# Kernel tuning notes

Hardware: AMD Instinct MI355X
Metric: run time of the kernel (lower is better)

## Reference

```python
import jax, jax.numpy as jnp
import numpy as np

HEADS = 12
D_MODEL = 768
D_K = D_MODEL // HEADS
BS, SEQ = 2, 4096


def setup_inputs() -> dict:
    key = jax.random.key(0)
    ks = jax.random.split(key, 12)
    s = 1.0 / np.sqrt(D_MODEL)
    return {
        "q": jax.random.normal(ks[0], (BS, SEQ, D_MODEL), jnp.float32),
        "k": jax.random.normal(ks[1], (BS, SEQ, D_MODEL), jnp.float32),
        "v": jax.random.normal(ks[2], (BS, SEQ, D_MODEL), jnp.float32),
        "Wq": jax.random.normal(ks[3], (D_MODEL, D_MODEL), jnp.float32) * s,
        "bq": jax.random.normal(ks[4], (D_MODEL,), jnp.float32) * s,
        "Wk": jax.random.normal(ks[5], (D_MODEL, D_MODEL), jnp.float32) * s,
        "bk": jax.random.normal(ks[6], (D_MODEL,), jnp.float32) * s,
        "Wv": jax.random.normal(ks[7], (D_MODEL, D_MODEL), jnp.float32) * s,
        "bv": jax.random.normal(ks[8], (D_MODEL,), jnp.float32) * s,
        "Wo": jax.random.normal(ks[9], (D_MODEL, D_MODEL), jnp.float32) * s,
        "bo": jax.random.normal(ks[10], (D_MODEL,), jnp.float32) * s,
        "mask": jnp.ones((BS, 1, SEQ), jnp.int32),
    }


def reference(q, k, v, Wq, bq, Wk, bk, Wv, bv, Wo, bo, mask):
    bs, sq, _ = q.shape
    # torch Linear: x @ W.T + b; then reshape to (bs, S, h, d_k) and transpose to (bs, h, S, d_k)
    def proj(x, W, b):
        y = x @ W.T + b
        return y.reshape(bs, -1, HEADS, D_K).transpose(0, 2, 1, 3)
    qh, kh, vh = proj(q, Wq, bq), proj(k, Wk, bk), proj(v, Wv, bv)
    scores = jnp.einsum("bhqd,bhkd->bhqk", qh, kh) / np.sqrt(D_K)
    # mask.unsqueeze(1): [bs,1,1,S_kv], masked_fill where mask == 0
    scores = jnp.where(mask[:, None, :, :] == 0, jnp.float32(-1e9), scores)
    attn = jax.nn.softmax(scores, axis=-1)  # dropout = identity (eval mode)
    ctx = jnp.einsum("bhqk,bhkd->bhqd", attn, vh)
    concat = ctx.transpose(0, 2, 1, 3).reshape(bs, sq, D_MODEL)
    return concat @ Wo.T + bo
```

## Files before the change

kernel.cpp:

```cpp
#include <hip/hip_runtime.h>
#include <hip/hip_bf16.h>

typedef __bf16 bf16x8 __attribute__((ext_vector_type(8)));
typedef __bf16 bf16x4 __attribute__((ext_vector_type(4)));
typedef float f32x4 __attribute__((ext_vector_type(4)));
typedef unsigned short u16;

#define HEADS 12
#define DK 64
#define DM 768
#define SEQL 4096
#define BSZ 2
#define MROWS (BSZ * SEQL)
#define WELEM (DM * DM)
#define NX 6291456
#define WTOT (4 * WELEM)
#define BTOT (4 * 768)

#define QSCALE 0.180336880434245f
#define EXP2F(x) __builtin_amdgcn_exp2f(x)

__device__ __forceinline__ float bf2f(u16 x) {
    unsigned int u = ((unsigned int)x) << 16;
    return __uint_as_float(u);
}
__device__ __forceinline__ u16 f2bf(float f) {
    unsigned int u = __float_as_uint(f);
    u += 0x7fff + ((u >> 16) & 1);
    return (u16)(u >> 16);
}
__device__ __forceinline__ unsigned int cvt_pk(float lo, float hi) {
#if __has_builtin(__builtin_amdgcn_cvt_pk_bf16_f32)
    auto r = __builtin_amdgcn_cvt_pk_bf16_f32(lo, hi);
    unsigned int u;
    __builtin_memcpy(&u, &r, 4);
    return u;
#else
    return (unsigned int)f2bf(lo) | ((unsigned int)f2bf(hi) << 16);
#endif
}

__global__ void detect_dtype(const u16* __restrict__ q, int* __restrict__ flag) {
    __shared__ int cnt;
    if (threadIdx.x == 0) cnt = 0;
    __syncthreads();
    int c = 0;
    for (int i = threadIdx.x; i < 16384; i += 256) {
        u16 x = q[i];
        if (((x >> 7) & 0xFF) == 0xFF) c++;
    }
    if (c) atomicAdd(&cnt, c);
    __syncthreads();
    if (threadIdx.x == 0) *flag = (cnt > 0) ? 1 : 0;
}

#define XBLKS (3 * NX / 8 / 256)
#define WBBLKS (((WTOT + BTOT) / 4 + 255) / 256)
__global__ __launch_bounds__(256) void convert_all(
    const void* __restrict__ X0, const void* __restrict__ X1, const void* __restrict__ X2,
    const void* __restrict__ W0, const void* __restrict__ W1,
    const void* __restrict__ W2, const void* __restrict__ W3,
    const void* __restrict__ B0, const void* __restrict__ B1,
    const void* __restrict__ B2, const void* __restrict__ B3,
    u16* __restrict__ Xc, u16* __restrict__ Wc, u16* __restrict__ bc,
    const int* __restrict__ flag) {
    const int f32m = *flag;
    if (blockIdx.x < XBLKS) {
        int i8 = blockIdx.x * 256 + threadIdx.x;
        int w = i8 / (NX / 8);
        int off8 = i8 - w * (NX / 8);
        const void* src = (w == 0) ? X0 : (w == 1) ? X1 : X2;
        u16* dst = Xc + (size_t)w * NX + (size_t)off8 * 8;
        if (f32m) {
            float4 f0 = ((const float4*)src)[off8 * 2];
            float4 f1 = ((const float4*)src)[off8 * 2 + 1];
            uint4 p = {cvt_pk(f0.x, f0.y), cvt_pk(f0.z, f0.w),
                       cvt_pk(f1.x, f1.y), cvt_pk(f1.z, f1.w)};
            *(uint4*)dst = p;
        } else {
            *(uint4*)dst = ((const uint4*)src)[off8];
        }
        return;
    }
    int i4 = (blockIdx.x - XBLKS) * 256 + threadIdx.x;
    const int n4 = (WTOT + BTOT) / 4;
    if (i4 >= n4) return;
    int base = i4 * 4;
    const void* src;
    u16* dst;
    int off;
    if (base < WTOT) {
        int w = base / WELEM;
        off = base - w * WELEM;
        src = (w == 0) ? W0 : (w == 1) ? W1 : (w == 2) ? W2 : W3;
        dst = Wc + w * WELEM + off;
    } else {
        int bi = base - WTOT;
        int w = bi / 768;
        off = bi - w * 768;
        src = (w == 0) ? B0 : (w == 1) ? B1 : (w == 2) ? B2 : B3;
        dst = bc + w * 768 + off;
    }
    if (f32m) {
        float4 f = *(const float4*)((const float*)src + off);
        uint2 p = {cvt_pk(f.x, f.y), cvt_pk(f.z, f.w)};
        *(uint2*)dst = p;
    } else {
        *(uint2*)dst = *(const uint2*)((const u16*)src + off);
    }
}

typedef __attribute__((address_space(1))) unsigned int glb_u32;
typedef __attribute__((address_space(3))) unsigned int lds_u32;

__device__ __forceinline__ void gld16(const u16* g, u16* l) {
    __builtin_amdgcn_global_load_lds((glb_u32*)g, (lds_u32*)l, 16, 0, 0);
}

template <int NCH>
__device__ __forceinline__ void stage_g(const u16* gbase, u16* lbase, int tid) {
#pragma unroll
    for (int it = 0; it < NCH / 256; ++it) {
        int c = it * 256 + tid;
        int row = c >> 2, p = c & 3;
        int gc = p ^ (row & 3);
        gld16(gbase + (size_t)row * DM + gc * 8, lbase + c * 8);
    }
}

__global__ __launch_bounds__(256) void gemm_qkv3(
    const u16* __restrict__ X0, const u16* __restrict__ X1, const u16* __restrict__ X2,
    const u16* __restrict__ Wc, const u16* __restrict__ bc,
    u16* __restrict__ Yq, u16* __restrict__ Yk, u16* __restrict__ Yv) {
    __shared__ __align__(16) u16 SM[2][2][128 * 32];

    const int L   = blockIdx.y * 64 + blockIdx.x;
    const int g   = L >> 3;
    const int bxn = (L & 7) * 8 + (g & 7);
    const int byn = g >> 3;

    const int sel = byn / 6;
    const int n0  = (byn - sel * 6) * 128;
    const int m0  = bxn * 128;

    const u16* X  = sel == 0 ? X0 : (sel == 1 ? X1 : X2);
    const u16* W  = Wc + (size_t)sel * WELEM;
    const u16* Bp = bc + sel * 768;
    u16* Y = sel == 0 ? Yq : (sel == 1 ? Yk : Yv);
    const float oscale = sel == 0 ? QSCALE : 1.0f;

    const int tid = threadIdx.x, lane = tid & 63, wave = tid >> 6;
    const int wr = (wave >> 1) * 64, wc2 = (wave & 1) * 64;
    const int l15 = lane & 15, quad = lane >> 4;
    const int ck = (quad ^ (l15 & 3)) * 8;

    f32x4 acc[4][4] = {};

    stage_g<512>(X + (size_t)m0 * DM, &SM[0][0][0], tid);
    stage_g<512>(W + (size_t)n0 * DM, &SM[1][0][0], tid);
    __syncthreads();

    for (int it = 0; it < 24; ++it) {
        const int cur = it & 1, nxt = cur ^ 1;
        if (it < 23) {
            stage_g<512>(X + (size_t)m0 * DM + (it + 1) * 32, &SM[0][nxt][0], tid);
            stage_g<512>(W + (size_t)n0 * DM + (it + 1) * 32, &SM[1][nxt][0], tid);
        }
        bf16x8 a[4], b[4];
#pragma unroll
        for (int i = 0; i < 4; ++i)
            a[i] = *(const bf16x8*)&SM[0][cur][(wr + i * 16 + l15) * 32 + ck];
#pragma unroll
        for (int j = 0; j < 4; ++j)
            b[j] = *(const bf16x8*)&SM[1][cur][(wc2 + j * 16 + l15) * 32 + ck];
        if (sel < 2) {
#pragma unroll
            for (int i = 0; i < 4; ++i)
#pragma unroll
                for (int j = 0; j < 4; ++j)
                    acc[i][j] = __builtin_amdgcn_mfma_f32_16x16x32_bf16(b[j], a[i], acc[i][j], 0, 0, 0);
        } else {
#pragma unroll
            for (int i = 0; i < 4; ++i)
#pragma unroll
                for (int j = 0; j < 4; ++j)
                    acc[i][j] = __builtin_amdgcn_mfma_f32_16x16x32_bf16(a[i], b[j], acc[i][j], 0, 0, 0);
        }
        __syncthreads();
    }

    u16* eb = &SM[0][0][0] + wave * 4096;
    const int r7l = l15 & 7;
    const int hh = (n0 + wc2) >> 6;

    if (sel < 2) {
        f32x4 bj[4];
#pragma unroll
        for (int j = 0; j < 4; ++j) {
            uint2 bb4 = *(const uint2*)&Bp[n0 + wc2 + j * 16 + quad * 4];
            bj[j][0] = bf2f((u16)(bb4.x & 0xffff));
            bj[j][1] = bf2f((u16)(bb4.x >> 16));
            bj[j][2] = bf2f((u16)(bb4.y & 0xffff));
            bj[j][3] = bf2f((u16)(bb4.y >> 16));
        }
#pragma unroll
        for (int i = 0; i < 4; ++i) {
            int Yl = i * 16 + l15;
#pragma unroll
            for (int j = 0; j < 4; ++j) {
                float v0 = (acc[i][j][0] + bj[j][0]) * oscale;
                float v1 = (acc[i][j][1] + bj[j][1]) * oscale;
                float v2 = (acc[i][j][2] + bj[j][2]) * oscale;
                float v3 = (acc[i][j][3] + bj[j][3]) * oscale;
                uint2 cv = {cvt_pk(v0, v1), cvt_pk(v2, v3)};
                int ch = (j * 4 + quad) ^ (r7l * 2);
                *(uint2*)&eb[Yl * 64 + ch * 4] = cv;
            }
        }
        asm volatile("" ::: "memory");
#pragma unroll
        for (int it2 = 0; it2 < 8; ++it2) {
            int Yp = it2 * 8 + (lane >> 3);
            int sc = ((lane & 7) * 2) ^ ((Yp & 7) * 2);
            uint4 w = *(const uint4*)&eb[Yp * 64 + sc * 4];
            int row0 = m0 + wr + Yp;
            int bb = row0 >> 12, s0 = row0 & (SEQL - 1);
            *(uint4*)&Y[(((size_t)(bb * HEADS + hh)) << 18) + (s0 << 6) + (lane & 7) * 8] = w;
        }
    } else {
#pragma unroll
        for (int j = 0; j < 4; ++j) {
            int Yl = j * 16 + l15;
            float bv = bf2f(Bp[n0 + wc2 + Yl]);
#pragma unroll
            for (int i = 0; i < 4; ++i) {
                uint2 cv = {cvt_pk(acc[i][j][0] + bv, acc[i][j][1] + bv),
                            cvt_pk(acc[i][j][2] + bv, acc[i][j][3] + bv)};
                int ch = (i * 4 + quad) ^ (r7l * 2);
                *(uint2*)&eb[Yl * 64 + ch * 4] = cv;
            }
        }
        asm volatile("" ::: "memory");
        const int bb = (m0 + wr) >> 12, s0 = (m0 + wr) & (SEQL - 1);
#pragma unroll
        for (int it2 = 0; it2 < 8; ++it2) {
            int Yp = it2 * 8 + (lane >> 3);
            int sc = ((lane & 7) * 2) ^ ((Yp & 7) * 2);
            uint4 w = *(const uint4*)&eb[Yp * 64 + sc * 4];
            *(uint4*)&Y[(((size_t)(bb * HEADS + hh)) << 18) + ((size_t)Yp << 12) + s0 + (lane & 7) * 8] = w;
        }
    }
}

__global__ __launch_bounds__(256) void gemm_out3(const u16* __restrict__ X,
                                                 const u16* __restrict__ W,
                                                 const u16* __restrict__ Bp,
                                                 void* __restrict__ Y,
                                                 const int* __restrict__ flag) {
    __shared__ __align__(16) u16 As[2][64 * 32];
    __shared__ __align__(16) u16 Bs[2][128 * 32];

    const int f32mode = *flag;
    const int L  = blockIdx.y * 128 + blockIdx.x;
    const int g  = L >> 3;
    const int m0 = ((L & 7) * 16 + (g & 15)) * 64;
    const int n0 = (g >> 4) * 128;
    const int tid = threadIdx.x, lane = tid & 63, wave = tid >> 6;
    const int wr = (wave >> 1) * 32, wc2 = (wave & 1) * 64;
    const int l15 = lane & 15, quad = lane >> 4;
    const int ck = (quad ^ (l15 & 3)) * 8;

    f32x4 acc[2][4] = {};

    stage_g<256>(X + (size_t)m0 * DM, &As[0][0], tid);
    stage_g<512>(W + (size_t)n0 * DM, &Bs[0][0], tid);
    __syncthreads();

    for (int it = 0; it < 24; ++it) {
        const int cur = it & 1, nxt = cur ^ 1;
        if (it < 23) {
            stage_g<256>(X + (size_t)m0 * DM + (it + 1) * 32, &As[nxt][0], tid);
            stage_g<512>(W + (size_t)n0 * DM + (it + 1) * 32, &Bs[nxt][0], tid);
        }
        bf16x8 a[2], b[4];
#pragma unroll
        for (int i = 0; i < 2; ++i)
            a[i] = *(const bf16x8*)&As[cur][(wr + i * 16 + l15) * 32 + ck];
#pragma unroll
        for (int j = 0; j < 4; ++j)
            b[j] = *(const bf16x8*)&Bs[cur][(wc2 + j * 16 + l15) * 32 + ck];
#pragma unroll
        for (int i = 0; i < 2; ++i)
#pragma unroll
            for (int j = 0; j < 4; ++j)
                acc[i][j] = __builtin_amdgcn_mfma_f32_16x16x32_bf16(a[i], b[j], acc[i][j], 0, 0, 0);
        __syncthreads();
    }

#pragma unroll
    for (int j = 0; j < 4; ++j) {
        int o = n0 + wc2 + j * 16 + l15;
        float bv = bf2f(Bp[o]);
#pragma unroll
        for (int i = 0; i < 2; ++i)
#pragma unroll
            for (int r = 0; r < 4; ++r) {
                int row = m0 + wr + i * 16 + quad * 4 + r;
                float val = acc[i][j][r] + bv;
                if (f32mode) ((float*)Y)[(size_t)row * DM + o] = val;
                else         ((u16*)Y)[(size_t)row * DM + o] = f2bf(val);
            }
    }
}

__device__ __forceinline__ void stage8_bf16(u16* dst, const u16* src) {
    *(uint4*)dst = *(const uint4*)src;
}
__device__ __forceinline__ void stage16_bf16(u16* dst, const u16* src) {
    *(uint4*)dst = *(const uint4*)src;
    *(uint4*)(dst + 8) = *(const uint4*)(src + 8);
}
__device__ __forceinline__ void stage16_f32pk(u16* dst, const float* src) {
    float4 f0 = ((const float4*)src)[0];
    float4 f1 = ((const float4*)src)[1];
    float4 f2 = ((const float4*)src)[2];
    float4 f3 = ((const float4*)src)[3];
    uint4 lo = {cvt_pk(f0.x, f0.y), cvt_pk(f0.z, f0.w), cvt_pk(f1.x, f1.y), cvt_pk(f1.z, f1.w)};
    uint4 hi = {cvt_pk(f2.x, f2.y), cvt_pk(f2.z, f2.w), cvt_pk(f3.x, f3.y), cvt_pk(f3.z, f3.w)};
    *(uint4*)dst = lo;
    *(uint4*)(dst + 8) = hi;
}

__global__ __launch_bounds__(256) void gemm_qkv_fb(
    const void* __restrict__ Xq, const void* __restrict__ Xk, const void* __restrict__ Xv,
    const u16* __restrict__ Wc, const u16* __restrict__ bc,
    u16* __restrict__ Yq, u16* __restrict__ Yk, u16* __restrict__ Yv,
    const int* __restrict__ flag) {
    __shared__ __align__(16) u16 As[128][40];
    __shared__ __align__(16) u16 Bs[64][40];
    const int f32mode = *flag;
    const int by = blockIdx.y;
    const int sel = by / 12;
    const int n0 = (by - sel * 12) * 64;
    const int m0 = blockIdx.x * 128;
    const void* Xp = sel == 0 ? Xq : (sel == 1 ? Xk : Xv);
    const u16* Wp = Wc + sel * WELEM;
    const u16* Bp = bc + sel * 768;
    u16* Y = sel == 0 ? Yq : (sel == 1 ? Yk : Yv);
    const float oscale = sel == 0 ? QSCALE : 1.0f;
    const int tid = threadIdx.x, lane = tid & 63, wave = tid >> 6;
    const int wr = (wave >> 1) * 64, wc = (wave & 1) * 32;
    const int l15 = lane & 15, quad = lane >> 4;
    const int srA = tid >> 1, scA = (tid & 1) * 16;
    const int srB = tid >> 2, scB = (tid & 3) * 8;
    f32x4 acc[4][2] = {};
    const size_t xoff = (size_t)(m0 + srA) * DM + scA;
    const size_t woff = (size_t)(n0 + srB) * DM + scB;
    for (int kb = 0; kb < DM; kb += 32) {
        if (f32mode) stage16_f32pk(&As[srA][scA], (const float*)Xp + xoff + kb);
        else         stage16_bf16(&As[srA][scA], (const u16*)Xp + xoff + kb);
        stage8_bf16(&Bs[srB][scB], Wp + woff + kb);
        __syncthreads();
        bf16x8 a[4], b[2];
#pragma unroll
        for (int i = 0; i < 4; ++i) a[i] = *(const bf16x8*)&As[wr + i * 16 + l15][quad * 8];
#pragma unroll
        for (int j = 0; j < 2; ++j) b[j] = *(const bf16x8*)&Bs[wc + j * 16 + l15][quad * 8];
#pragma unroll
        for (int i = 0; i < 4; ++i)
#pragma unroll
            for (int j = 0; j < 2; ++j)
                acc[i][j] = __builtin_amdgcn_mfma_f32_16x16x32_bf16(a[i], b[j], acc[i][j], 0, 0, 0);
        __syncthreads();
    }
#pragma unroll
    for (int j = 0; j < 2; ++j) {
        int o = n0 + wc + j * 16 + l15;
        float bv = bf2f(Bp[o]);
#pragma unroll
        for (int i = 0; i < 4; ++i)
#pragma unroll
            for (int r = 0; r < 4; ++r) {
                int row = m0 + wr + i * 16 + quad * 4 + r;
                float val = (acc[i][j][r] + bv) * oscale;
                int bb = row >> 12, s = row & (SEQL - 1);
                int h = o >> 6, d = o & 63;
                if (sel < 2) Y[((bb * HEADS + h) << 18) + (s << 6) + d] = f2bf(val);
                else         Y[((bb * HEADS + h) << 18) + (d << 12) + s] = f2bf(val);
            }
    }
}

__global__ __launch_bounds__(256) void gemm_out_fb(const u16* __restrict__ X,
                                                   const u16* __restrict__ Wp,
                                                   const u16* __restrict__ Bp,
                                                   void* __restrict__ Y,
                                                   const int* __restrict__ flag) {
    __shared__ __align__(16) u16 As[128][40];
    __shared__ __align__(16) u16 Bs[64][40];
    const int f32mode = *flag;
    const int m0 = blockIdx.x * 128, n0 = blockIdx.y * 64;
    const int tid = threadIdx.x, lane = tid & 63, wave = tid >> 6;
    const int wr = (wave >> 1) * 64, wc = (wave & 1) * 32;
    const int l15 = lane & 15, quad = lane >> 4;
    const int srA = tid >> 1, scA = (tid & 1) * 16;
    const int srB = tid >> 2, scB = (tid & 3) * 8;
    f32x4 acc[4][2] = {};
    const size_t xoff = (size_t)(m0 + srA) * DM + scA;
    const size_t woff = (size_t)(n0 + srB) * DM + scB;
    for (int kb = 0; kb < DM; kb += 32) {
        stage16_bf16(&As[srA][scA], X + xoff + kb);
        stage8_bf16(&Bs[srB][scB], Wp + woff + kb);
        __syncthreads();
        bf16x8 a[4], b[2];
#pragma unroll
        for (int i = 0; i < 4; ++i) a[i] = *(const bf16x8*)&As[wr + i * 16 + l15][quad * 8];
#pragma unroll
        for (int j = 0; j < 2; ++j) b[j] = *(const bf16x8*)&Bs[wc + j * 16 + l15][quad * 8];
#pragma unroll
        for (int i = 0; i < 4; ++i)
#pragma unroll
            for (int j = 0; j < 2; ++j)
                acc[i][j] = __builtin_amdgcn_mfma_f32_16x16x32_bf16(a[i], b[j], acc[i][j], 0, 0, 0);
        __syncthreads();
    }
#pragma unroll
    for (int j = 0; j < 2; ++j) {
        int o = n0 + wc + j * 16 + l15;
        float bv = bf2f(Bp[o]);
#pragma unroll
        for (int i = 0; i < 4; ++i)
#pragma unroll
            for (int r = 0; r < 4; ++r) {
                int row = m0 + wr + i * 16 + quad * 4 + r;
                float val = acc[i][j][r] + bv;
                if (f32mode) ((float*)Y)[(size_t)row * DM + o] = val;
                else         ((u16*)Y)[(size_t)row * DM + o] = f2bf(val);
            }
    }
}

__device__ __forceinline__ void stage_tile(const u16* gbase, int rstride,
                                           u16* lbase, int tid) {
#pragma unroll
    for (int it = 0; it < 2; ++it) {
        int c = it * 256 + tid;
        int row = c >> 3, p = c & 7;
        int gc = p ^ (row & 7);
        gld16(gbase + (size_t)row * rstride + gc * 8, lbase + c * 8);
    }
}

__global__ __launch_bounds__(256, 3) void flash_attn(const u16* __restrict__ Q,
                                                     const u16* __restrict__ K,
                                                     const u16* __restrict__ Vt,
                                                     const int* __restrict__ mask,
                                                     u16* __restrict__ ctx) {
    __shared__ __align__(16) u16 KVs[2][2][64 * 64];
    __shared__ __align__(16) float Ms[2][64];
    __shared__ int Mf[2];
    __shared__ int AnyM;

    const int tid  = threadIdx.x;
    const int lane = tid & 63;
    const int wave = tid >> 6;
    const int l15  = lane & 15;
    const int quad = lane >> 4;

    const int L  = blockIdx.y * 32 + blockIdx.x;
    const int gg = L >> 3;
    const int bh = (L & 7) * 3 + (gg >> 5);
    const int qblk = gg & 31;

    const int b  = bh / HEADS;
    const int h  = bh - b * HEADS;
    const int qb = qblk * 128 + wave * 32;

    const u16* Qh = Q  + ((size_t)bh << 18);
    const u16* Kh = K  + ((size_t)bh << 18);
    const u16* Vh = Vt + ((size_t)bh << 18);
    const int* maskb = mask + b * SEQL;

    if (tid == 0) AnyM = 0;
    int zf = 0;
#pragma unroll
    for (int i = 0; i < 16; ++i) zf |= (maskb[tid + i * 256] == 0);

    bf16x8 aq[2][2];
#pragma unroll
    for (int s = 0; s < 2; ++s)
#pragma unroll
        for (int c = 0; c < 2; ++c)
            aq[s][c] = *(const bf16x8*)&Qh[(size_t)(qb + s * 16 + l15) * DK + c * 32 + quad * 8];

    __syncthreads();
    if (zf) atomicOr(&AnyM, 1);
    __syncthreads();
    const int anym = AnyM;

    const int r7   = l15 & 7;
    const int ck0  = (quad ^ r7) * 8;
    const int ck1  = ((quad + 4) ^ r7) * 8;
    const int lrow = l15 * 64;
    const int vq   = quad >> 1;
    const int voff = (quad & 1) * 4;

    f32x4 o_acc[2][4] = {};
    f32x4 l_acc[2] = {};

    bf16x8 aones;
    {
        unsigned int w1 = 0x3F803F80u;
        uint4 o4 = {w1, w1, w1, w1};
        __builtin_memcpy(&aones, &o4, 16);
    }

    stage_tile(Kh, DK, &KVs[0][0][0], tid);
    stage_tile(Vh, SEQL, &KVs[0][1][0], tid);
    int mreg = 0;
    if (anym && tid < 64) {
        mreg = maskb[tid];
        int anyt = __any(mreg == 0);
        Ms[0][tid] = (mreg == 0) ? -1.0e9f : 0.0f;
        if (tid == 0) Mf[0] = anyt;
        mreg = maskb[64 + tid];
    }
    __syncthreads();

#pragma unroll 2
    for (int t = 0; t < 64; ++t) {
        const int cur = t & 1, nxt = cur ^ 1;
        if (t < 63) {
            const int kt = (t + 1) * 64;
            stage_tile(Kh + (size_t)kt * DK, DK, &KVs[nxt][0][0], tid);
            stage_tile(Vh + kt, SEQL, &KVs[nxt][1][0], tid);
            if (anym && tid < 64) {
                int anyt = __any(mreg == 0);
                Ms[nxt][tid] = (mreg == 0) ? -1.0e9f : 0.0f;
                if (tid == 0) Mf[nxt] = anyt;
                if (t < 62) mreg = maskb[(t + 2) * 64 + tid];
            }
        }

        const u16* kb2 = &KVs[cur][0][0];
        const u16* vb  = &KVs[cur][1][0];

        f32x4 s4[2][4];
#pragma unroll
        for (int nt = 0; nt < 4; ++nt) {
            bf16x8 ak0 = *(const bf16x8*)&kb2[lrow + nt * 1024 + ck0];
            bf16x8 ak1 = *(const bf16x8*)&kb2[lrow + nt * 1024 + ck1];
#pragma unroll
            for (int s = 0; s < 2; ++s) {
                f32x4 z = {};
                z = __builtin_amdgcn_mfma_f32_16x16x32_bf16(ak0, aq[s][0], z, 0, 0, 0);
                z = __builtin_amdgcn_mfma_f32_16x16x32_bf16(ak1, aq[s][1], z, 0, 0, 0);
                s4[s][nt] = z;
            }
        }
        const int usebias = anym ? Mf[cur] : 0;
        if (usebias) {
#pragma unroll
            for (int nt = 0; nt < 4; ++nt) {
                f32x4 bias = *(const f32x4*)&Ms[cur][nt * 16 + quad * 4];
#pragma unroll
                for (int s = 0; s < 2; ++s)
#pragma unroll
                    for (int r = 0; r < 4; ++r) s4[s][nt][r] += bias[r];
            }
        }

#pragma unroll
        for (int s = 0; s < 2; ++s)
#pragma unroll
            for (int nt = 0; nt < 4; ++nt) {
                s4[s][nt][0] = EXP2F(s4[s][nt][0]);
                s4[s][nt][1] = EXP2F(s4[s][nt][1]);
                s4[s][nt][2] = EXP2F(s4[s][nt][2]);
                s4[s][nt][3] = EXP2F(s4[s][nt][3]);
            }

        bf16x8 pp[2][2];
#pragma unroll
        for (int s = 0; s < 2; ++s)
#pragma unroll
            for (int kbi = 0; kbi < 2; ++kbi) {
                uint4 cv = {cvt_pk(s4[s][2 * kbi][0],     s4[s][2 * kbi][1]),
                            cvt_pk(s4[s][2 * kbi][2],     s4[s][2 * kbi][3]),
                            cvt_pk(s4[s][2 * kbi + 1][0], s4[s][2 * kbi + 1][1]),
                            cvt_pk(s4[s][2 * kbi + 1][2], s4[s][2 * kbi + 1][3])};
                __builtin_memcpy(&pp[s][kbi], &cv, 16);
            }

        bf16x8 av[4][2];
#pragma unroll
        for (int dv = 0; dv < 4; ++dv) {
            const u16* vr = &vb[(dv * 16 + l15) * 64];
#pragma unroll
            for (int kbi = 0; kbi < 2; ++kbi) {
                uint2 lo = *(const uint2*)&vr[((kbi * 4 + vq) ^ r7) * 8 + voff];
                uint2 hi = *(const uint2*)&vr[((kbi * 4 + 2 + vq) ^ r7) * 8 + voff];
                uint4 cc = {lo.x, lo.y, hi.x, hi.y};
                __builtin_memcpy(&av[dv][kbi], &cc, 16);
            }
        }

        __builtin_amdgcn_s_setprio(1);
#pragma unroll
        for (int kbi = 0; kbi < 2; ++kbi) {
#pragma unroll
            for (int dv = 0; dv < 4; ++dv)
#pragma unroll
                for (int s = 0; s < 2; ++s)
                    o_acc[s][dv] = __builtin_amdgcn_mfma_f32_16x16x32_bf16(
                        av[dv][kbi], pp[s][kbi], o_acc[s][dv], 0, 0, 0);
#pragma unroll
            for (int s = 0; s < 2; ++s)
                l_acc[s] = __builtin_amdgcn_mfma_f32_16x16x32_bf16(
                    aones, pp[s][kbi], l_acc[s], 0, 0, 0);
        }
        __builtin_amdgcn_s_setprio(0);
        __syncthreads();
    }

    u16* eb = &KVs[0][0][0] + wave * 2304;
#pragma unroll
    for (int s = 0; s < 2; ++s) {
        float inv = 1.0f / l_acc[s][0];
#pragma unroll
        for (int dv = 0; dv < 4; ++dv) {
            uint2 cv = {cvt_pk(o_acc[s][dv][0] * inv, o_acc[s][dv][1] * inv),
                        cvt_pk(o_acc[s][dv][2] * inv, o_acc[s][dv][3] * inv)};
            *(uint2*)&eb[(s * 16 + l15) * 72 + dv * 16 + quad * 4] = cv;
        }
    }
    asm volatile("" ::: "memory");
    {
        int rowq = lane >> 2, dchunk = lane & 3;
#pragma unroll
        for (int s = 0; s < 2; ++s) {
            uint4 w0 = *(const uint4*)&eb[(s * 16 + rowq) * 72 + dchunk * 16];
            uint4 w1 = *(const uint4*)&eb[(s * 16 + rowq) * 72 + dchunk * 16 + 8];
            size_t orow = (size_t)(b * SEQL + qb + s * 16 + rowq) * DM + h * DK + dchunk * 16;
            *(uint4*)&ctx[orow] = w0;
            *(uint4*)&ctx[orow + 8] = w1;
        }
    }
}

extern "C" void kernel_launch(void* const* d_in, const int* in_sizes, int n_in,
                              void* d_out, int out_size, void* d_ws, size_t ws_size,
                              hipStream_t stream) {
    const void* q   = d_in[0];
    const void* k   = d_in[1];
    const void* v   = d_in[2];
    const void* Wq  = d_in[3];
    const void* bq  = d_in[4];
    const void* Wk  = d_in[5];
    const void* bk  = d_in[6];
    const void* Wv  = d_in[7];
    const void* bv  = d_in[8];
    const void* Wo  = d_in[9];
    const void* bo  = d_in[10];
    const int* mask = (const int*)d_in[11];

    const size_t NSH = (size_t)NX;
    u16* ws = (u16*)d_ws;

    const size_t need_full = (6 * NSH + WTOT + BTOT) * sizeof(u16) + 64;
    const size_t need_fb   = (4 * NSH + WTOT + BTOT) * sizeof(u16) + 64;

    if (ws_size >= need_full) {
        u16* Qh  = ws;
        u16* Kh  = ws + NSH;
        u16* Vth = ws + 2 * NSH;
        u16* Xc  = ws + 3 * NSH;
        u16* ctx = Xc;
        u16* Wc  = ws + 6 * NSH;
        u16* bc  = Wc + WTOT;
        int* dflag = (int*)(bc + BTOT);

        detect_dtype<<<1, 256, 0, stream>>>((const u16*)q, dflag);
        convert_all<<<XBLKS + WBBLKS, 256, 0, stream>>>(
            q, k, v, Wq, Wk, Wv, Wo, bq, bk, bv, bo, Xc, Wc, bc, dflag);

        gemm_qkv3<<<dim3(MROWS / 128, 18), 256, 0, stream>>>(
            Xc, Xc + NSH, Xc + 2 * NSH, Wc, bc, Qh, Kh, Vth);
        flash_attn<<<dim3(SEQL / 128, BSZ * HEADS), 256, 0, stream>>>(Qh, Kh, Vth, mask, ctx);
        gemm_out3<<<dim3(MROWS / 64, 6), 256, 0, stream>>>(
            ctx, Wc + 3 * (size_t)WELEM, bc + 3 * 768, d_out, dflag);
    } else if (ws_size >= need_fb) {
        u16* Qh  = ws;
        u16* Kh  = ws + NSH;
        u16* Vth = ws + 2 * NSH;
        u16* ctx = ws + 3 * NSH;
        u16* Wc  = ws + 4 * NSH;
        u16* bc  = Wc + WTOT;
        int* dflag = (int*)(bc + BTOT);

        detect_dtype<<<1, 256, 0, stream>>>((const u16*)q, dflag);
        convert_all<<<XBLKS + WBBLKS, 256, 0, stream>>>(
            q, k, v, Wq, Wk, Wv, Wo, bq, bk, bv, bo, Qh , Wc, bc, dflag);
        gemm_qkv_fb<<<dim3(MROWS / 128, 36), 256, 0, stream>>>(
            q, k, v, Wc, bc, Qh, Kh, Vth, dflag);
        flash_attn<<<dim3(SEQL / 128, BSZ * HEADS), 256, 0, stream>>>(Qh, Kh, Vth, mask, ctx);
        gemm_out_fb<<<dim3(MROWS / 128, 12), 256, 0, stream>>>(
            ctx, Wc + 3 * (size_t)WELEM, bc + 3 * 768, d_out, dflag);
    }
}
```

Before: 349.5 us.

## Fuse fp32-to-bf16 activation conversion into QKV projection GEMM staging

Removes the separate pass that converted the q/k/v activations to bf16 in workspace. The QKV GEMM now loads fp32 rows straight from the inputs into registers, converts them to bf16 after the MFMA work of each step, and writes them to LDS; the bf16 path keeps the direct global-to-LDS loads. This avoids writing and re-reading about 37 MB of intermediate activations. In exchange, fp32 input traffic goes through registers instead of the async LDS load path, and the fallback kernels and workspace branch are deleted.

```diff
diff --git a/kernel.cpp b/kernel.cpp
--- a/kernel.cpp
+++ b/kernel.cpp
@@ -54,35 +54,15 @@
     if (threadIdx.x == 0) *flag = (cnt > 0) ? 1 : 0;
 }
 
-#define XBLKS (3 * NX / 8 / 256)
 #define WBBLKS (((WTOT + BTOT) / 4 + 255) / 256)
-__global__ __launch_bounds__(256) void convert_all(
-    const void* __restrict__ X0, const void* __restrict__ X1, const void* __restrict__ X2,
+__global__ __launch_bounds__(256) void convert_wb(
     const void* __restrict__ W0, const void* __restrict__ W1,
     const void* __restrict__ W2, const void* __restrict__ W3,
     const void* __restrict__ B0, const void* __restrict__ B1,
     const void* __restrict__ B2, const void* __restrict__ B3,
-    u16* __restrict__ Xc, u16* __restrict__ Wc, u16* __restrict__ bc,
-    const int* __restrict__ flag) {
+    u16* __restrict__ Wc, u16* __restrict__ bc, const int* __restrict__ flag) {
     const int f32m = *flag;
-    if (blockIdx.x < XBLKS) {
-        int i8 = blockIdx.x * 256 + threadIdx.x;
-        int w = i8 / (NX / 8);
-        int off8 = i8 - w * (NX / 8);
-        const void* src = (w == 0) ? X0 : (w == 1) ? X1 : X2;
-        u16* dst = Xc + (size_t)w * NX + (size_t)off8 * 8;
-        if (f32m) {
-            float4 f0 = ((const float4*)src)[off8 * 2];
-            float4 f1 = ((const float4*)src)[off8 * 2 + 1];
-            uint4 p = {cvt_pk(f0.x, f0.y), cvt_pk(f0.z, f0.w),
-                       cvt_pk(f1.x, f1.y), cvt_pk(f1.z, f1.w)};
-            *(uint4*)dst = p;
-        } else {
-            *(uint4*)dst = ((const uint4*)src)[off8];
-        }
-        return;
-    }
-    int i4 = (blockIdx.x - XBLKS) * 256 + threadIdx.x;
+    int i4 = blockIdx.x * 256 + threadIdx.x;
     const int n4 = (WTOT + BTOT) / 4;
     if (i4 >= n4) return;
     int base = i4 * 4;
@@ -129,10 +109,13 @@
 }
 
 __global__ __launch_bounds__(256) void gemm_qkv3(
-    const u16* __restrict__ X0, const u16* __restrict__ X1, const u16* __restrict__ X2,
+    const void* __restrict__ X0r, const void* __restrict__ X1r, const void* __restrict__ X2r,
     const u16* __restrict__ Wc, const u16* __restrict__ bc,
-    u16* __restrict__ Yq, u16* __restrict__ Yk, u16* __restrict__ Yv) {
+    u16* __restrict__ Yq, u16* __restrict__ Yk, u16* __restrict__ Yv,
+    const int* __restrict__ flag) {
     __shared__ __align__(16) u16 SM[2][2][128 * 32];
+
+    const int f32m = *flag;
 
     const int L   = blockIdx.y * 64 + blockIdx.x;
     const int g   = L >> 3;
@@ -143,7 +126,7 @@
     const int n0  = (byn - sel * 6) * 128;
     const int m0  = bxn * 128;
 
-    const u16* X  = sel == 0 ? X0 : (sel == 1 ? X1 : X2);
+    const void* Xr = sel == 0 ? X0r : (sel == 1 ? X1r : X2r);
     const u16* W  = Wc + (size_t)sel * WELEM;
     const u16* Bp = bc + sel * 768;
     u16* Y = sel == 0 ? Yq : (sel == 1 ? Yk : Yv);
@@ -154,17 +137,47 @@
     const int l15 = lane & 15, quad = lane >> 4;
     const int ck = (quad ^ (l15 & 3)) * 8;
 
+    const int c0 = tid,        r0 = c0 >> 2, g0 = (c0 & 3) ^ (r0 & 3);
+    const int c1 = 256 + tid,  r1 = c1 >> 2, g1 = (c1 & 3) ^ (r1 & 3);
+
+    const float* Xf = (const float*)Xr;
+    const u16*   Xh = (const u16*)Xr;
+
     f32x4 acc[4][4] = {};
 
-    stage_g<512>(X + (size_t)m0 * DM, &SM[0][0][0], tid);
+    if (f32m) {
+        const float* s0 = Xf + (size_t)(m0 + r0) * DM + g0 * 8;
+        const float* s1 = Xf + (size_t)(m0 + r1) * DM + g1 * 8;
+        float4 a0 = ((const float4*)s0)[0], b0 = ((const float4*)s0)[1];
+        float4 a1 = ((const float4*)s1)[0], b1 = ((const float4*)s1)[1];
+        uint4 p0 = {cvt_pk(a0.x, a0.y), cvt_pk(a0.z, a0.w),
+                    cvt_pk(b0.x, b0.y), cvt_pk(b0.z, b0.w)};
+        uint4 p1 = {cvt_pk(a1.x, a1.y), cvt_pk(a1.z, a1.w),
+                    cvt_pk(b1.x, b1.y), cvt_pk(b1.z, b1.w)};
+        *(uint4*)(&SM[0][0][0] + c0 * 8) = p0;
+        *(uint4*)(&SM[0][0][0] + c1 * 8) = p1;
+    } else {
+        gld16(Xh + (size_t)(m0 + r0) * DM + g0 * 8, &SM[0][0][0] + c0 * 8);
+        gld16(Xh + (size_t)(m0 + r1) * DM + g1 * 8, &SM[0][0][0] + c1 * 8);
+    }
     stage_g<512>(W + (size_t)n0 * DM, &SM[1][0][0], tid);
     __syncthreads();
 
     for (int it = 0; it < 24; ++it) {
         const int cur = it & 1, nxt = cur ^ 1;
+        float4 pa0, pb0, pa1, pb1;
         if (it < 23) {
-            stage_g<512>(X + (size_t)m0 * DM + (it + 1) * 32, &SM[0][nxt][0], tid);
-            stage_g<512>(W + (size_t)n0 * DM + (it + 1) * 32, &SM[1][nxt][0], tid);
+            const int kb = (it + 1) * 32;
+            if (f32m) {
+                const float* s0 = Xf + (size_t)(m0 + r0) * DM + kb + g0 * 8;
+                const float* s1 = Xf + (size_t)(m0 + r1) * DM + kb + g1 * 8;
+                pa0 = ((const float4*)s0)[0]; pb0 = ((const float4*)s0)[1];
+                pa1 = ((const float4*)s1)[0]; pb1 = ((const float4*)s1)[1];
+            } else {
+                gld16(Xh + (size_t)(m0 + r0) * DM + kb + g0 * 8, &SM[0][nxt][0] + c0 * 8);
+                gld16(Xh + (size_t)(m0 + r1) * DM + kb + g1 * 8, &SM[0][nxt][0] + c1 * 8);
+            }
+            stage_g<512>(W + (size_t)n0 * DM + kb, &SM[1][nxt][0], tid);
         }
         bf16x8 a[4], b[4];
 #pragma unroll
@@ -185,6 +198,14 @@
 #pragma unroll
                 for (int j = 0; j < 4; ++j)
                     acc[i][j] = __builtin_amdgcn_mfma_f32_16x16x32_bf16(a[i], b[j], acc[i][j], 0, 0, 0);
+        }
+        if (it < 23 && f32m) {
+            uint4 p0 = {cvt_pk(pa0.x, pa0.y), cvt_pk(pa0.z, pa0.w),
+                        cvt_pk(pb0.x, pb0.y), cvt_pk(pb0.z, pb0.w)};
+            uint4 p1 = {cvt_pk(pa1.x, pa1.y), cvt_pk(pa1.z, pa1.w),
+                        cvt_pk(pb1.x, pb1.y), cvt_pk(pb1.z, pb1.w)};
+            *(uint4*)(&SM[0][nxt][0] + c0 * 8) = p0;
+            *(uint4*)(&SM[0][nxt][0] + c1 * 8) = p1;
         }
         __syncthreads();
     }
@@ -303,133 +324,6 @@
         float bv = bf2f(Bp[o]);
 #pragma unroll
         for (int i = 0; i < 2; ++i)
-#pragma unroll
-            for (int r = 0; r < 4; ++r) {
-                int row = m0 + wr + i * 16 + quad * 4 + r;
-                float val = acc[i][j][r] + bv;
-                if (f32mode) ((float*)Y)[(size_t)row * DM + o] = val;
-                else         ((u16*)Y)[(size_t)row * DM + o] = f2bf(val);
-            }
-    }
-}
-
-__device__ __forceinline__ void stage8_bf16(u16* dst, const u16* src) {
-    *(uint4*)dst = *(const uint4*)src;
-}
-__device__ __forceinline__ void stage16_bf16(u16* dst, const u16* src) {
-    *(uint4*)dst = *(const uint4*)src;
-    *(uint4*)(dst + 8) = *(const uint4*)(src + 8);
-}
-__device__ __forceinline__ void stage16_f32pk(u16* dst, const float* src) {
-    float4 f0 = ((const float4*)src)[0];
-    float4 f1 = ((const float4*)src)[1];
-    float4 f2 = ((const float4*)src)[2];
-    float4 f3 = ((const float4*)src)[3];
-    uint4 lo = {cvt_pk(f0.x, f0.y), cvt_pk(f0.z, f0.w), cvt_pk(f1.x, f1.y), cvt_pk(f1.z, f1.w)};
-    uint4 hi = {cvt_pk(f2.x, f2.y), cvt_pk(f2.z, f2.w), cvt_pk(f3.x, f3.y), cvt_pk(f3.z, f3.w)};
-    *(uint4*)dst = lo;
-    *(uint4*)(dst + 8) = hi;
-}
-
-__global__ __launch_bounds__(256) void gemm_qkv_fb(
-    const void* __restrict__ Xq, const void* __restrict__ Xk, const void* __restrict__ Xv,
-    const u16* __restrict__ Wc, const u16* __restrict__ bc,
-    u16* __restrict__ Yq, u16* __restrict__ Yk, u16* __restrict__ Yv,
-    const int* __restrict__ flag) {
-    __shared__ __align__(16) u16 As[128][40];
-    __shared__ __align__(16) u16 Bs[64][40];
-    const int f32mode = *flag;
-    const int by = blockIdx.y;
-    const int sel = by / 12;
-    const int n0 = (by - sel * 12) * 64;
-    const int m0 = blockIdx.x * 128;
-    const void* Xp = sel == 0 ? Xq : (sel == 1 ? Xk : Xv);
-    const u16* Wp = Wc + sel * WELEM;
-    const u16* Bp = bc + sel * 768;
-    u16* Y = sel == 0 ? Yq : (sel == 1 ? Yk : Yv);
-    const float oscale = sel == 0 ? QSCALE : 1.0f;
-    const int tid = threadIdx.x, lane = tid & 63, wave = tid >> 6;
-    const int wr = (wave >> 1) * 64, wc = (wave & 1) * 32;
-    const int l15 = lane & 15, quad = lane >> 4;
-    const int srA = tid >> 1, scA = (tid & 1) * 16;
-    const int srB = tid >> 2, scB = (tid & 3) * 8;
-    f32x4 acc[4][2] = {};
-    const size_t xoff = (size_t)(m0 + srA) * DM + scA;
-    const size_t woff = (size_t)(n0 + srB) * DM + scB;
-    for (int kb = 0; kb < DM; kb += 32) {
-        if (f32mode) stage16_f32pk(&As[srA][scA], (const float*)Xp + xoff + kb);
-        else         stage16_bf16(&As[srA][scA], (const u16*)Xp + xoff + kb);
-        stage8_bf16(&Bs[srB][scB], Wp + woff + kb);
-        __syncthreads();
-        bf16x8 a[4], b[2];
-#pragma unroll
-        for (int i = 0; i < 4; ++i) a[i] = *(const bf16x8*)&As[wr + i * 16 + l15][quad * 8];
-#pragma unroll
-        for (int j = 0; j < 2; ++j) b[j] = *(const bf16x8*)&Bs[wc + j * 16 + l15][quad * 8];
-#pragma unroll
-        for (int i = 0; i < 4; ++i)
-#pragma unroll
-            for (int j = 0; j < 2; ++j)
-                acc[i][j] = __builtin_amdgcn_mfma_f32_16x16x32_bf16(a[i], b[j], acc[i][j], 0, 0, 0);
-        __syncthreads();
-    }
-#pragma unroll
-    for (int j = 0; j < 2; ++j) {
-        int o = n0 + wc + j * 16 + l15;
-        float bv = bf2f(Bp[o]);
-#pragma unroll
-        for (int i = 0; i < 4; ++i)
-#pragma unroll
-            for (int r = 0; r < 4; ++r) {
-                int row = m0 + wr + i * 16 + quad * 4 + r;
-                float val = (acc[i][j][r] + bv) * oscale;
-                int bb = row >> 12, s = row & (SEQL - 1);
-                int h = o >> 6, d = o & 63;
-                if (sel < 2) Y[((bb * HEADS + h) << 18) + (s << 6) + d] = f2bf(val);
-                else         Y[((bb * HEADS + h) << 18) + (d << 12) + s] = f2bf(val);
-            }
-    }
-}
-
-__global__ __launch_bounds__(256) void gemm_out_fb(const u16* __restrict__ X,
-                                                   const u16* __restrict__ Wp,
-                                                   const u16* __restrict__ Bp,
-                                                   void* __restrict__ Y,
-                                                   const int* __restrict__ flag) {
-    __shared__ __align__(16) u16 As[128][40];
-    __shared__ __align__(16) u16 Bs[64][40];
-    const int f32mode = *flag;
-    const int m0 = blockIdx.x * 128, n0 = blockIdx.y * 64;
-    const int tid = threadIdx.x, lane = tid & 63, wave = tid >> 6;
-    const int wr = (wave >> 1) * 64, wc = (wave & 1) * 32;
-    const int l15 = lane & 15, quad = lane >> 4;
-    const int srA = tid >> 1, scA = (tid & 1) * 16;
-    const int srB = tid >> 2, scB = (tid & 3) * 8;
-    f32x4 acc[4][2] = {};
-    const size_t xoff = (size_t)(m0 + srA) * DM + scA;
-    const size_t woff = (size_t)(n0 + srB) * DM + scB;
-    for (int kb = 0; kb < DM; kb += 32) {
-        stage16_bf16(&As[srA][scA], X + xoff + kb);
-        stage8_bf16(&Bs[srB][scB], Wp + woff + kb);
-        __syncthreads();
-        bf16x8 a[4], b[2];
-#pragma unroll
-        for (int i = 0; i < 4; ++i) a[i] = *(const bf16x8*)&As[wr + i * 16 + l15][quad * 8];
-#pragma unroll
-        for (int j = 0; j < 2; ++j) b[j] = *(const bf16x8*)&Bs[wc + j * 16 + l15][quad * 8];
-#pragma unroll
-        for (int i = 0; i < 4; ++i)
-#pragma unroll
-            for (int j = 0; j < 2; ++j)
-                acc[i][j] = __builtin_amdgcn_mfma_f32_16x16x32_bf16(a[i], b[j], acc[i][j], 0, 0, 0);
-        __syncthreads();
-    }
-#pragma unroll
-    for (int j = 0; j < 2; ++j) {
-        int o = n0 + wc + j * 16 + l15;
-        float bv = bf2f(Bp[o]);
-#pragma unroll
-        for (int i = 0; i < 4; ++i)
 #pragma unroll
             for (int r = 0; r < 4; ++r) {
                 int row = m0 + wr + i * 16 + quad * 4 + r;
@@ -667,44 +561,24 @@
     const size_t NSH = (size_t)NX;
     u16* ws = (u16*)d_ws;
 
-    const size_t need_full = (6 * NSH + WTOT + BTOT) * sizeof(u16) + 64;
-    const size_t need_fb   = (4 * NSH + WTOT + BTOT) * sizeof(u16) + 64;
-
-    if (ws_size >= need_full) {
-        u16* Qh  = ws;
-        u16* Kh  = ws + NSH;
-        u16* Vth = ws + 2 * NSH;
-        u16* Xc  = ws + 3 * NSH;
-        u16* ctx = Xc;
-        u16* Wc  = ws + 6 * NSH;
-        u16* bc  = Wc + WTOT;
-        int* dflag = (int*)(bc + BTOT);
-
-        detect_dtype<<<1, 256, 0, stream>>>((const u16*)q, dflag);
-        convert_all<<<XBLKS + WBBLKS, 256, 0, stream>>>(
-            q, k, v, Wq, Wk, Wv, Wo, bq, bk, bv, bo, Xc, Wc, bc, dflag);
-
-        gemm_qkv3<<<dim3(MROWS / 128, 18), 256, 0, stream>>>(
-            Xc, Xc + NSH, Xc + 2 * NSH, Wc, bc, Qh, Kh, Vth);
-        flash_attn<<<dim3(SEQL / 128, BSZ * HEADS), 256, 0, stream>>>(Qh, Kh, Vth, mask, ctx);
-        gemm_out3<<<dim3(MROWS / 64, 6), 256, 0, stream>>>(
-            ctx, Wc + 3 * (size_t)WELEM, bc + 3 * 768, d_out, dflag);
-    } else if (ws_size >= need_fb) {
-        u16* Qh  = ws;
-        u16* Kh  = ws + NSH;
-        u16* Vth = ws + 2 * NSH;
-        u16* ctx = ws + 3 * NSH;
-        u16* Wc  = ws + 4 * NSH;
-        u16* bc  = Wc + WTOT;
-        int* dflag = (int*)(bc + BTOT);
-
-        detect_dtype<<<1, 256, 0, stream>>>((const u16*)q, dflag);
-        convert_all<<<XBLKS + WBBLKS, 256, 0, stream>>>(
-            q, k, v, Wq, Wk, Wv, Wo, bq, bk, bv, bo, Qh , Wc, bc, dflag);
-        gemm_qkv_fb<<<dim3(MROWS / 128, 36), 256, 0, stream>>>(
-            q, k, v, Wc, bc, Qh, Kh, Vth, dflag);
-        flash_attn<<<dim3(SEQL / 128, BSZ * HEADS), 256, 0, stream>>>(Qh, Kh, Vth, mask, ctx);
-        gemm_out_fb<<<dim3(MROWS / 128, 12), 256, 0, stream>>>(
-            ctx, Wc + 3 * (size_t)WELEM, bc + 3 * 768, d_out, dflag);
-    }
-}
+    const size_t need = (4 * NSH + WTOT + BTOT) * sizeof(u16) + 64;
+    if (ws_size < need) return;
+
+    u16* Qh  = ws;
+    u16* Kh  = ws + NSH;
+    u16* Vth = ws + 2 * NSH;
+    u16* ctx = ws + 3 * NSH;
+    u16* Wc  = ws + 4 * NSH;
+    u16* bc  = Wc + WTOT;
+    int* dflag = (int*)(bc + BTOT);
+
+    detect_dtype<<<1, 256, 0, stream>>>((const u16*)q, dflag);
+    convert_wb<<<WBBLKS, 256, 0, stream>>>(
+        Wq, Wk, Wv, Wo, bq, bk, bv, bo, Wc, bc, dflag);
+
+    gemm_qkv3<<<dim3(MROWS / 128, 18), 256, 0, stream>>>(
+        q, k, v, Wc, bc, Qh, Kh, Vth, dflag);
+    flash_attn<<<dim3(SEQL / 128, BSZ * HEADS), 256, 0, stream>>>(Qh, Kh, Vth, mask, ctx);
+    gemm_out3<<<dim3(MROWS / 64, 6), 256, 0, stream>>>(
+        ctx, Wc + 3 * (size_t)WELEM, bc + 3 * 768, d_out, dflag);
+}
```

Result: slower. 374.6 us (+7.2%).
